# Optimization experiments

Hardware: AMD Instinct MI355X
Metric: run time of the kernel (lower is better)

Reference implementation:

```python
import jax, jax.numpy as jnp
import numpy as np

HIDDEN = 3072
N_HEADS = 16
Q_LORA = 1536
KV_LORA = 512
NOPE = 128
ROPE = 64
QK_HD = NOPE + ROPE  # 192
V_HD = 128
B, S = 2, 1024


def rms_norm(x, w, eps=1e-6):
    xf = x.astype(jnp.float32)
    var = jnp.mean(xf * xf, axis=-1, keepdims=True)
    return w * (xf * jax.lax.rsqrt(var + eps)).astype(x.dtype)


def apply_rope(x):
    # x: (b, s, h, d) with d even; interleaved pair rotation as in the source
    b, s, h, d = x.shape
    pos = jnp.arange(s, dtype=jnp.float32)
    inv_freq = 1.0 / (10000.0 ** (jnp.arange(0, d, 2, dtype=jnp.float32) / d))
    ang = pos[:, None] * inv_freq[None, :]          # (s, d/2)
    sin = jnp.sin(ang)[None, :, None, :]            # (1, s, 1, d/2)
    cos = jnp.cos(ang)[None, :, None, :]
    xr = x.reshape(b, s, h, d // 2, 2)
    x1, x2 = xr[..., 0], xr[..., 1]
    r1 = x1 * cos - x2 * sin
    r2 = x1 * sin + x2 * cos
    return jnp.stack([r1, r2], axis=-1).reshape(b, s, h, d)


def setup_inputs() -> dict:
    key = jax.random.key(0)
    ks = jax.random.split(key, 16)
    sc = 0.02
    inp = {
        "hidden_states": jax.random.normal(ks[0], (B, S, HIDDEN), jnp.float32),
        # causal additive mask (s, t): 0 on/below diagonal, -1e9 above
        "mask": jnp.where(jnp.tril(jnp.ones((S, S), bool)), 0.0, -1e9).astype(jnp.float32),
        "wq_a_w": jax.random.normal(ks[1], (Q_LORA, HIDDEN), jnp.float32) * sc,
        "wq_a_b": jnp.zeros((Q_LORA,), jnp.float32),
        "q_norm_w": jnp.ones((Q_LORA,), jnp.float32),
        "wq_b_w": jax.random.normal(ks[2], (HIDDEN, Q_LORA), jnp.float32) * sc,
        "wq_b_b": jnp.zeros((HIDDEN,), jnp.float32),
        "wkv_a_w": jax.random.normal(ks[3], (KV_LORA + ROPE, HIDDEN), jnp.float32) * sc,
        "wkv_a_b": jnp.zeros((KV_LORA + ROPE,), jnp.float32),
        "kv_norm_w": jnp.ones((KV_LORA,), jnp.float32),
        "wkv_b_w": jax.random.normal(ks[4], (N_HEADS * (NOPE + V_HD), KV_LORA), jnp.float32) * sc,
        "wkv_b_b": jnp.zeros((N_HEADS * (NOPE + V_HD),), jnp.float32),
        "wo_w": jax.random.normal(ks[5], (HIDDEN, N_HEADS * V_HD), jnp.float32) * sc,
        "wo_b": jnp.zeros((HIDDEN,), jnp.float32),
    }
    return inp


def reference(hidden_states, mask, wq_a_w, wq_a_b, q_norm_w, wq_b_w, wq_b_b,
              wkv_a_w, wkv_a_b, kv_norm_w, wkv_b_w, wkv_b_b, wo_w, wo_b):
    b, s, _ = hidden_states.shape
    scale = QK_HD ** (-0.5)

    # low-rank Q projection
    q_lat = hidden_states @ wq_a_w.T + wq_a_b                  # (b,s,q_lora)
    q = rms_norm(q_lat, q_norm_w) @ wq_b_w.T + wq_b_b          # (b,s,hidden)
    q = q.reshape(b, s, N_HEADS, QK_HD)
    q_nope, q_rope = q[..., :NOPE], q[..., NOPE:]
    q_rope = apply_rope(q_rope)
    q = jnp.concatenate([q_nope, q_rope], axis=-1)             # (b,s,h,192)

    # low-rank KV projection with decoupled rope key
    kv = hidden_states @ wkv_a_w.T + wkv_a_b                   # (b,s,kv_lora+rope)
    kv_lat, k_rope = kv[..., :KV_LORA], kv[..., KV_LORA:]
    k_rope = apply_rope(k_rope[:, :, None, :])                 # (b,s,1,64)
    kv = rms_norm(kv_lat, kv_norm_w) @ wkv_b_w.T + wkv_b_b
    kv = kv.reshape(b, s, N_HEADS, NOPE + V_HD)
    k_nope, v = kv[..., :NOPE], kv[..., NOPE:]
    k = jnp.concatenate([k_nope, jnp.broadcast_to(k_rope, (b, s, N_HEADS, ROPE))], axis=-1)

    # naive full attention, fp32 softmax (as in source)
    scores = jnp.einsum('bshd,bthd->bsht', q, k) * scale       # (b,s,h,t)
    scores = scores + mask[None, :, None, :]
    p = jax.nn.softmax(scores.astype(jnp.float32), axis=-1)
    out = jnp.einsum('bsht,bthd->bshd', p, v)                  # (b,s,h,v_hd)
    out = out.reshape(b, s, N_HEADS * V_HD)
    return out @ wo_w.T + wo_b
```

## Files before the change

### kernel.cpp

```cpp
#include <hip/hip_runtime.h>
#include <stdint.h>
#include <stddef.h>

#define NHEADS 16
#define QLORA  1536
#define KVLORA 512
#define QKH    192
#define VH     128
#define BB     2
#define SS     1024
#define MROWS  (BB*SS)
#define HID    3072

typedef __attribute__((ext_vector_type(4))) float fx4;
typedef __attribute__((ext_vector_type(4))) short sx4;
typedef __attribute__((ext_vector_type(8))) short sx8;

__device__ __forceinline__ short f2bf(float f) {
  uint32_t u = __builtin_bit_cast(uint32_t, f);
  u = (u + 0x7fffu + ((u >> 16) & 1u)) >> 16;
  return (short)u;
}
__device__ __forceinline__ float bf2f(short s) {
  uint32_t u = ((uint32_t)(uint16_t)s) << 16;
  return __builtin_bit_cast(float, u);
}
__device__ __forceinline__ void gl_lds16(const void* g, void* l) {
  __builtin_amdgcn_global_load_lds((const __attribute__((address_space(1))) void*)g,
                                   (__attribute__((address_space(3))) void*)l, 16, 0, 0);
}
__device__ __forceinline__ sx8 ldfrag(const short* p) {
  sx4 lo = *(const sx4*)p;
  sx4 hi = *(const sx4*)(p + 16);
  sx8 r;
  r[0]=lo[0]; r[1]=lo[1]; r[2]=lo[2]; r[3]=lo[3];
  r[4]=hi[0]; r[5]=hi[1]; r[6]=hi[2]; r[7]=hi[3];
  return r;
}
__device__ __forceinline__ sx8 ldfrag_swz(const short* lds, int row, int rowShorts,
                                          int baseChunk, int g) {
  const int r7 = row & 7;
  const int gh = g >> 1, lo4 = (g & 1) * 4;
  int ch0 = baseChunk + gh;
  int ch1 = baseChunk + 2 + gh;
  ch0 = (ch0 & ~7) | ((ch0 & 7) ^ r7);
  ch1 = (ch1 & ~7) | ((ch1 & 7) ^ r7);
  const short* base = lds + row * rowShorts;
  sx4 a = *(const sx4*)(base + ch0 * 8 + lo4);
  sx4 b = *(const sx4*)(base + ch1 * 8 + lo4);
  sx8 r;
  r[0]=a[0]; r[1]=a[1]; r[2]=a[2]; r[3]=a[3];
  r[4]=b[0]; r[5]=b[1]; r[6]=b[2]; r[7]=b[3];
  return r;
}

struct CvtSeg { const float* src; short* dst; int n4; };
__global__ void k_cvt6(CvtSeg s0, CvtSeg s1, CvtSeg s2, CvtSeg s3, CvtSeg s4, CvtSeg s5) {
  const CvtSeg segs[6] = {s0, s1, s2, s3, s4, s5};
  const int stride = gridDim.x * blockDim.x;
  const int t0 = blockIdx.x * blockDim.x + threadIdx.x;
#pragma unroll
  for (int s = 0; s < 6; ++s) {
    const float* src = segs[s].src;
    short* dst = segs[s].dst;
    const int n4 = segs[s].n4;
    for (int i = t0; i < n4; i += stride) {
      fx4 v = *(const fx4*)(src + (size_t)i * 4);
      sx4 o;
      o[0] = f2bf(v[0]); o[1] = f2bf(v[1]); o[2] = f2bf(v[2]); o[3] = f2bf(v[3]);
      *(sx4*)(dst + (size_t)i * 4) = o;
    }
  }
}

__global__ void k_rope_tab(float* __restrict__ tab) {
  int i = blockIdx.x * blockDim.x + threadIdx.x;
  if (i >= SS * 32) return;
  int pos = i >> 5, fi = i & 31;
  float inv = powf(10000.0f, -(float)fi / 32.0f);
  float ang = (float)pos * inv;
  tab[i * 2]     = cosf(ang);
  tab[i * 2 + 1] = sinf(ang);
}

struct GemmProb {
  const short* A; const short* Bt; const float* bias; void* C;
  int N; int K;
};

template <int SPLITK>
__global__ __launch_bounds__(256, 4)
void k_gemmS(GemmProb p0, GemmProb p1, int nblk0) {
  int nwg = gridDim.x;
  int bid = (blockIdx.x % 8) * (nwg >> 3) + (blockIdx.x >> 3);
  const GemmProb p = (bid < nblk0) ? p0 : p1;
  int lb = (bid < nblk0) ? bid : bid - nblk0;
  const int N = p.N, K = p.K;
  const int NT = (N + 127) >> 7;
  const int tiles = 16 * NT;
  const int tile = lb % tiles;
  const int pi = (SPLITK > 1) ? (lb / tiles) : 0;
  const int m0 = (tile % 16) * 128;
  const int n0 = (tile / 16) * 128;
  const int Kc = K / SPLITK;
  const int k0 = pi * Kc;

  __shared__ short As[128 * 64];
  __shared__ short Bs[128 * 64];
  const int tid  = threadIdx.x;
  const int lane = tid & 63;
  const int g    = lane >> 4;
  const int r16  = lane & 15;
  const int wave = tid >> 6;
  const int wm   = (wave >> 1) * 64;
  const int wn   = (wave & 1) * 64;

  fx4 acc[4][4] = {};

  for (int kk = k0; kk < k0 + Kc; kk += 64) {
#pragma unroll
    for (int i = 0; i < 4; ++i) {
      int cc  = tid + 256 * i;
      int row = cc >> 3;
      int src = ((cc & 7) ^ (row & 7)) * 8;
      int bn = n0 + row; if (bn > N - 1) bn = N - 1;
      gl_lds16(p.A + (size_t)(m0 + row) * K + kk + src, &As[cc * 8]);
      gl_lds16(p.Bt + (size_t)bn * K + kk + src, &Bs[cc * 8]);
    }
    __syncthreads();

#pragma unroll
    for (int s = 0; s < 2; ++s) {
      sx8 af[4], bfv[4];
#pragma unroll
      for (int mi = 0; mi < 4; ++mi)
        af[mi] = ldfrag_swz(As, wm + mi * 16 + r16, 64, s * 4, g);
#pragma unroll
      for (int ni = 0; ni < 4; ++ni)
        bfv[ni] = ldfrag_swz(Bs, wn + ni * 16 + r16, 64, s * 4, g);
#pragma unroll
      for (int mi = 0; mi < 4; ++mi)
#pragma unroll
        for (int ni = 0; ni < 4; ++ni)
          acc[mi][ni] = __builtin_amdgcn_mfma_f32_16x16x32_bf16(af[mi], bfv[ni], acc[mi][ni], 0, 0, 0);
    }
    __syncthreads();
  }

  if (SPLITK > 1) {
    float* Cp = (float*)p.C + (size_t)pi * 2048 * N;
#pragma unroll
    for (int mi = 0; mi < 4; ++mi) {
      int mbase = m0 + wm + mi * 16 + 4 * g;
#pragma unroll
      for (int ni = 0; ni < 4; ++ni) {
        int ncol = n0 + wn + ni * 16 + r16;
        if (ncol < N) {
#pragma unroll
          for (int r = 0; r < 4; ++r)
            Cp[(size_t)(mbase + r) * N + ncol] = acc[mi][ni][r];
        }
      }
    }
  } else {
#pragma unroll
    for (int mi = 0; mi < 4; ++mi) {
      int mbase = m0 + wm + mi * 16 + 4 * g;
#pragma unroll
      for (int ni = 0; ni < 4; ++ni) {
        int ncol = n0 + wn + ni * 16 + r16;
        if (ncol < N) {
          float bv = p.bias[ncol];
#pragma unroll
          for (int r = 0; r < 4; ++r)
            ((short*)p.C)[(size_t)(mbase + r) * N + ncol] = f2bf(acc[mi][ni][r] + bv);
        }
      }
    }
  }
}

__global__ __launch_bounds__(256)
void k_prep(const float* __restrict__ qp, const float* __restrict__ q_bias,
            const float* __restrict__ q_norm_w, short* __restrict__ qn,
            const float* __restrict__ kvp, const float* __restrict__ kv_bias,
            const float* __restrict__ kv_norm_w, short* __restrict__ kvn,
            short* __restrict__ kr, const float* __restrict__ tab) {
  const int row = blockIdx.x;
  const int t = threadIdx.x;
  const size_t QS = (size_t)2048 * QLORA;
  const size_t KS = (size_t)2048 * 576;

  float x[8];
  float s1 = 0.f, s2 = 0.f;
  if (t < 192) {
    const float* a = qp + (size_t)row * QLORA + t * 8;
    fx4 u0 = *(const fx4*)(a),          u1 = *(const fx4*)(a + 4);
    fx4 v0 = *(const fx4*)(a + QS),     v1 = *(const fx4*)(a + QS + 4);
    fx4 w0 = *(const fx4*)(a + 2 * QS), w1 = *(const fx4*)(a + 2 * QS + 4);
#pragma unroll
    for (int j = 0; j < 4; ++j) {
      x[j]     = u0[j] + v0[j] + w0[j] + q_bias[t * 8 + j];
      x[4 + j] = u1[j] + v1[j] + w1[j] + q_bias[t * 8 + 4 + j];
    }
#pragma unroll
    for (int j = 0; j < 8; ++j) s1 += x[j] * x[j];
  } else {
    const int c = t - 192;
    const float* a = kvp + (size_t)row * 576 + c * 8;
    fx4 u0 = *(const fx4*)(a),          u1 = *(const fx4*)(a + 4);
    fx4 v0 = *(const fx4*)(a + KS),     v1 = *(const fx4*)(a + KS + 4);
    fx4 w0 = *(const fx4*)(a + 2 * KS), w1 = *(const fx4*)(a + 2 * KS + 4);
#pragma unroll
    for (int j = 0; j < 4; ++j) {
      x[j]     = u0[j] + v0[j] + w0[j] + kv_bias[c * 8 + j];
      x[4 + j] = u1[j] + v1[j] + w1[j] + kv_bias[c * 8 + 4 + j];
    }
#pragma unroll
    for (int j = 0; j < 8; ++j) s2 += x[j] * x[j];
  }
#pragma unroll
  for (int o = 32; o >= 1; o >>= 1) {
    s1 += __shfl_xor(s1, o, 64);
    s2 += __shfl_xor(s2, o, 64);
  }
  __shared__ float r1[4], r2[4];
  if ((t & 63) == 0) { r1[t >> 6] = s1; r2[t >> 6] = s2; }
  __syncthreads();
  float qss = r1[0] + r1[1] + r1[2] + r1[3];
  float kss = r2[0] + r2[1] + r2[2] + r2[3];
  float qrs = 1.0f / sqrtf(qss / (float)QLORA + 1e-6f);
  float krs = 1.0f / sqrtf(kss / (float)KVLORA + 1e-6f);

  if (t < 192) {
    sx8 o;
#pragma unroll
    for (int j = 0; j < 8; ++j) o[j] = f2bf(x[j] * qrs * q_norm_w[t * 8 + j]);
    *(sx8*)(qn + (size_t)row * QLORA + t * 8) = o;
  } else {
    int c = t - 192;
    sx8 o;
#pragma unroll
    for (int j = 0; j < 8; ++j) o[j] = f2bf(x[j] * krs * kv_norm_w[c * 8 + j]);
    *(sx8*)(kvn + (size_t)row * KVLORA + c * 8) = o;
  }
  if (t < 8) {
    const float* a = kvp + (size_t)row * 576 + 512 + t * 8;
    fx4 u0 = *(const fx4*)(a),          u1 = *(const fx4*)(a + 4);
    fx4 v0 = *(const fx4*)(a + KS),     v1 = *(const fx4*)(a + KS + 4);
    fx4 w0 = *(const fx4*)(a + 2 * KS), w1 = *(const fx4*)(a + 2 * KS + 4);
    float y[8];
#pragma unroll
    for (int j = 0; j < 4; ++j) {
      y[j]     = u0[j] + v0[j] + w0[j] + kv_bias[512 + t * 8 + j];
      y[4 + j] = u1[j] + v1[j] + w1[j] + kv_bias[512 + t * 8 + 4 + j];
    }
    int pos = row & (SS - 1);
    sx8 o;
#pragma unroll
    for (int k = 0; k < 4; ++k) {
      int i = t * 4 + k;
      float c = tab[(pos * 32 + i) * 2], s = tab[(pos * 32 + i) * 2 + 1];
      o[2 * k]     = f2bf(y[2 * k] * c - y[2 * k + 1] * s);
      o[2 * k + 1] = f2bf(y[2 * k] * s + y[2 * k + 1] * c);
    }
    *(sx8*)(kr + (size_t)row * 64 + t * 8) = o;
  }
}

__global__ __launch_bounds__(256)
void k_post(const short* __restrict__ kvb, short* __restrict__ vt,
            short* __restrict__ qb, const float* __restrict__ tab) {
  const int bid = blockIdx.x;
  const int tid = threadIdx.x;
  if (bid < 512) {
    const int bh = bid >> 4;
    const int t0 = (bid & 15) * 64;
    const int b = bh >> 4, h = bh & 15;
    __shared__ short sm[64 * 128];
#pragma unroll
    for (int i = 0; i < 4; ++i) {
      int c = tid + 256 * i;
      int tt = c >> 4, d0 = (c & 15) * 8;
      sx8 v = *(const sx8*)(kvb + ((size_t)(b * SS + t0 + tt)) * 4096 + h * 256 + 128 + d0);
      *(sx8*)(sm + tt * 128 + d0) = v;
    }
    __syncthreads();
#pragma unroll
    for (int i = 0; i < 4; ++i) {
      int c = tid + 256 * i;
      int d = c >> 3, tof = (c & 7) * 8;
      sx8 v;
#pragma unroll
      for (int j = 0; j < 8; ++j) v[j] = sm[(tof + j) * 128 + d];
      *(sx8*)(vt + ((size_t)bh * VH + d) * SS + t0 + tof) = v;
    }
  } else {
    int p = (bid - 512) * 256 + tid;
    int j = p & 7, h = (p >> 3) & 15, row = p >> 7;
    int pos = row & (SS - 1);
    size_t base = (((size_t)row * NHEADS + h) * QKH) + 128 + j * 8;
    sx8 x = *(const sx8*)(qb + base);
    sx8 o;
#pragma unroll
    for (int k = 0; k < 4; ++k) {
      int i = j * 4 + k;
      float c = tab[(pos * 32 + i) * 2], s = tab[(pos * 32 + i) * 2 + 1];
      float x1 = bf2f(x[2 * k]), x2 = bf2f(x[2 * k + 1]);
      o[2 * k]     = f2bf(x1 * c - x2 * s);
      o[2 * k + 1] = f2bf(x1 * s + x2 * c);
    }
    *(sx8*)(qb + base) = o;
  }
}

__global__ __launch_bounds__(256)
void k_osum(const float* __restrict__ p, const float* __restrict__ bias,
            float* __restrict__ out) {
  const size_t OS = (size_t)2048 * HID;
  int i = blockIdx.x * 256 + threadIdx.x;
  fx4 a = *(const fx4*)(p + (size_t)i * 4);
  fx4 b = *(const fx4*)(p + OS + (size_t)i * 4);
  int col = (i * 4) % HID;
  fx4 bv = *(const fx4*)(bias + col);
  fx4 o = a + b + bv;
  *(fx4*)(out + (size_t)i * 4) = o;
}

__global__ __launch_bounds__(256, 2)
void k_attn(const short* __restrict__ q, const short* __restrict__ kvb,
            const short* __restrict__ kr, const short* __restrict__ vt,
            short* __restrict__ ao) {
  const int bh = blockIdx.x;
  const int b = bh >> 4, h = bh & 15;
  const int qt0 = blockIdx.y * 64;
  const int tid = threadIdx.x;
  const int lane = tid & 63;
  const int wave = tid >> 6;
  const int g = lane >> 4, r16 = lane & 15;
  const int qg = qt0 + wave * 16 + r16;

  __shared__ short Ks[64 * QKH];
  __shared__ short Vs[VH * 64];

  sx8 qf[6];
  {
    const short* qr = q + (((size_t)(b * SS + qg)) * NHEADS + h) * QKH;
#pragma unroll
    for (int f = 0; f < 6; ++f) qf[f] = ldfrag(qr + f * 32 + 4 * g);
  }

  float mrun = -1e30f, lrun = 0.0f;
  fx4 oacc[8] = {};
  const float scale = 0.07216878364870323f;

  const int ntiles = qt0 / 64 + 1;
  for (int kt = 0; kt < ntiles; ++kt) {
    const int t0 = kt * 64;
#pragma unroll
    for (int i = 0; i < 6; ++i) {
      int cc = tid + 256 * i;
      int row = cc / 24, ch = cc % 24;
      int sc = (ch & 24) | ((ch & 7) ^ (row & 7));
      size_t grow = (size_t)(b * SS + t0 + row);
      const short* src = (sc < 16) ? kvb + grow * 4096 + h * 256 + sc * 8
                                   : kr + grow * 64 + (sc - 16) * 8;
      gl_lds16(src, &Ks[cc * 8]);
    }
#pragma unroll
    for (int i = 0; i < 4; ++i) {
      int cc = tid + 256 * i;
      int row = cc >> 3;
      int sc = (cc & 7) ^ (row & 7);
      gl_lds16(vt + ((size_t)bh * VH + row) * SS + t0 + sc * 8, &Vs[cc * 8]);
    }
    __syncthreads();

    const bool diag = (kt == ntiles - 1);
    float pv[16];
    float tmax = -1e30f;
#pragma unroll
    for (int th = 0; th < 4; ++th) {
      fx4 sacc = {};
#pragma unroll
      for (int f = 0; f < 6; ++f) {
        sx8 kf = ldfrag_swz(Ks, th * 16 + r16, QKH, f * 4, g);
        sacc = __builtin_amdgcn_mfma_f32_16x16x32_bf16(kf, qf[f], sacc, 0, 0, 0);
      }
#pragma unroll
      for (int r = 0; r < 4; ++r) {
        int t = t0 + th * 16 + 4 * g + r;
        float s = sacc[r] * scale;
        if (diag && t > qg) s = -1e30f;
        pv[th * 4 + r] = s;
        tmax = fmaxf(tmax, s);
      }
    }
    tmax = fmaxf(tmax, __shfl_xor(tmax, 16, 64));
    tmax = fmaxf(tmax, __shfl_xor(tmax, 32, 64));
    float mnew = fmaxf(mrun, tmax);
    float corr = __expf(mrun - mnew);
    float psum = 0.f;
#pragma unroll
    for (int j = 0; j < 16; ++j) { pv[j] = __expf(pv[j] - mnew); psum += pv[j]; }
    psum += __shfl_xor(psum, 16, 64);
    psum += __shfl_xor(psum, 32, 64);
    lrun = lrun * corr + psum;
    mrun = mnew;
#pragma unroll
    for (int f8 = 0; f8 < 8; ++f8) oacc[f8] *= corr;

    sx8 pf0, pf1;
#pragma unroll
    for (int j = 0; j < 8; ++j) { pf0[j] = f2bf(pv[j]); pf1[j] = f2bf(pv[8 + j]); }

#pragma unroll
    for (int f8 = 0; f8 < 8; ++f8) {
      sx8 v0 = ldfrag_swz(Vs, f8 * 16 + r16, 64, 0, g);
      sx8 v1 = ldfrag_swz(Vs, f8 * 16 + r16, 64, 4, g);
      oacc[f8] = __builtin_amdgcn_mfma_f32_16x16x32_bf16(v0, pf0, oacc[f8], 0, 0, 0);
      oacc[f8] = __builtin_amdgcn_mfma_f32_16x16x32_bf16(v1, pf1, oacc[f8], 0, 0, 0);
    }
    __syncthreads();
  }

  float inv = 1.0f / lrun;
#pragma unroll
  for (int f8 = 0; f8 < 8; ++f8)
#pragma unroll
    for (int r = 0; r < 4; ++r) {
      int d = f8 * 16 + 4 * g + r;
      ao[(((size_t)(b * SS + qg)) * NHEADS + h) * VH + d] = f2bf(oacc[f8][r] * inv);
    }
}

extern "C" void kernel_launch(void* const* d_in, const int* in_sizes, int n_in,
                              void* d_out, int out_size, void* d_ws, size_t ws_size,
                              hipStream_t stream) {
  const float* hs       = (const float*)d_in[0];
  const float* wq_a_w   = (const float*)d_in[2];
  const float* wq_a_b   = (const float*)d_in[3];
  const float* q_norm_w = (const float*)d_in[4];
  const float* wq_b_w   = (const float*)d_in[5];
  const float* wq_b_b   = (const float*)d_in[6];
  const float* wkv_a_w  = (const float*)d_in[7];
  const float* wkv_a_b  = (const float*)d_in[8];
  const float* kv_norm_w= (const float*)d_in[9];
  const float* wkv_b_w  = (const float*)d_in[10];
  const float* wkv_b_b  = (const float*)d_in[11];
  const float* wo_w     = (const float*)d_in[12];
  const float* wo_b     = (const float*)d_in[13];
  float* out = (float*)d_out;

  short* ws0 = (short*)d_ws;
  size_t off = 0;
  short* wqa_bf  = ws0 + off; off += (size_t)QLORA * HID;
  short* wqb_bf  = ws0 + off; off += (size_t)HID * QLORA;
  short* wkva_bf = ws0 + off; off += (size_t)576 * HID;
  short* wkvb_bf = ws0 + off; off += (size_t)4096 * KVLORA;
  short* wo_bf   = ws0 + off; off += (size_t)HID * 2048;
  short* h_bf    = ws0 + off; off += (size_t)MROWS * HID;
  short* qn      = ws0 + off; off += (size_t)MROWS * QLORA;
  short* kvn     = ws0 + off; off += (size_t)MROWS * KVLORA;
  short* kr      = ws0 + off; off += (size_t)MROWS * 64;
  short* qb      = ws0 + off; off += (size_t)MROWS * HID;
  short* kvb     = ws0 + off; off += (size_t)MROWS * 4096;
  short* vtb     = ws0 + off; off += (size_t)BB * NHEADS * VH * SS;
  short* ao      = ws0 + off; off += (size_t)MROWS * 2048;
  float* tab     = (float*)(ws0 + off + (off & 1));
  float* arena   = tab + SS * 64;
  float* qlatp   = arena;
  float* kvp     = arena + (size_t)3 * 2048 * QLORA;
  float* wop     = arena;

  {
    CvtSeg s0{wq_a_w,  wqa_bf,  (int)((size_t)QLORA * HID / 4)};
    CvtSeg s1{wq_b_w,  wqb_bf,  (int)((size_t)HID * QLORA / 4)};
    CvtSeg s2{wkv_a_w, wkva_bf, (int)((size_t)576 * HID / 4)};
    CvtSeg s3{wkv_b_w, wkvb_bf, (int)((size_t)4096 * KVLORA / 4)};
    CvtSeg s4{wo_w,    wo_bf,   (int)((size_t)HID * 2048 / 4)};
    CvtSeg s5{hs,      h_bf,    (int)((size_t)MROWS * HID / 4)};
    k_cvt6<<<2048, 256, 0, stream>>>(s0, s1, s2, s3, s4, s5);
  }
  k_rope_tab<<<(SS * 32 + 255) / 256, 256, 0, stream>>>(tab);

  {
    GemmProb pq{h_bf, wqa_bf,  nullptr, qlatp, QLORA, HID};
    GemmProb pk{h_bf, wkva_bf, nullptr, kvp,   576,   HID};
    int nb0 = 16 * (QLORA / 128) * 3;
    int nb1 = 16 * ((576 + 127) / 128) * 3;
    k_gemmS<3><<<nb0 + nb1, 256, 0, stream>>>(pq, pk, nb0);
  }

  k_prep<<<MROWS, 256, 0, stream>>>(qlatp, wq_a_b, q_norm_w, qn,
                                    kvp, wkv_a_b, kv_norm_w, kvn, kr, tab);

  {
    GemmProb pq{qn,  wqb_bf,  wq_b_b,  qb,  HID,  QLORA};
    GemmProb pk{kvn, wkvb_bf, wkv_b_b, kvb, 4096, KVLORA};
    int nb0 = 16 * (HID / 128);
    int nb1 = 16 * (4096 / 128);
    k_gemmS<1><<<nb0 + nb1, 256, 0, stream>>>(pq, pk, nb0);
  }

  k_post<<<512 + 1024, 256, 0, stream>>>(kvb, vtb, qb, tab);

  k_attn<<<dim3(BB * NHEADS, SS / 64), 256, 0, stream>>>(qb, kvb, kr, vtb, ao);

  {
    GemmProb po{ao, wo_bf, nullptr, wop, HID, 2048};
    int nb = 16 * (HID / 128) * 2;
    k_gemmS<2><<<nb, 256, 0, stream>>>(po, po, nb);
  }
  k_osum<<<(MROWS * HID / 4) / 256, 256, 0, stream>>>(wop, wo_b, out);
}
```

Before: 250.9 us.

## Replace GEMM with 256x256-tile, 8-wave, double-buffered LDS pipelined kernel

```diff
diff --git a/kernel.cpp b/kernel.cpp
--- a/kernel.cpp
+++ b/kernel.cpp
@@ -89,92 +89,145 @@
 };
 
 template <int SPLITK>
-__global__ __launch_bounds__(256, 4)
-void k_gemmS(GemmProb p0, GemmProb p1, int nblk0) {
+__global__ __launch_bounds__(512, 2)
+void k_g8(GemmProb p0, GemmProb p1, int nblk0) {
   int nwg = gridDim.x;
   int bid = (blockIdx.x % 8) * (nwg >> 3) + (blockIdx.x >> 3);
   const GemmProb p = (bid < nblk0) ? p0 : p1;
   int lb = (bid < nblk0) ? bid : bid - nblk0;
   const int N = p.N, K = p.K;
-  const int NT = (N + 127) >> 7;
-  const int tiles = 16 * NT;
+  const int NT = N >> 8;
+  const int tiles = 8 * NT;
   const int tile = lb % tiles;
   const int pi = (SPLITK > 1) ? (lb / tiles) : 0;
-  const int m0 = (tile % 16) * 128;
-  const int n0 = (tile / 16) * 128;
+  const int m0 = (tile & 7) * 256;
+  const int n0 = (tile >> 3) * 256;
   const int Kc = K / SPLITK;
   const int k0 = pi * Kc;
 
-  __shared__ short As[128 * 64];
-  __shared__ short Bs[128 * 64];
+  __shared__ short lds[2][4][128 * 64];
+
   const int tid  = threadIdx.x;
   const int lane = tid & 63;
+  const int wave = tid >> 6;
+  const int wr   = wave >> 2;
+  const int wc   = wave & 3;
   const int g    = lane >> 4;
   const int r16  = lane & 15;
-  const int wave = tid >> 6;
-  const int wm   = (wave >> 1) * 64;
-  const int wn   = (wave & 1) * 64;
-
-  fx4 acc[4][4] = {};
-
-  for (int kk = k0; kk < k0 + Kc; kk += 64) {
-#pragma unroll
-    for (int i = 0; i < 4; ++i) {
-      int cc  = tid + 256 * i;
-      int row = cc >> 3;
-      int src = ((cc & 7) ^ (row & 7)) * 8;
-      int bn = n0 + row; if (bn > N - 1) bn = N - 1;
-      gl_lds16(p.A + (size_t)(m0 + row) * K + kk + src, &As[cc * 8]);
-      gl_lds16(p.Bt + (size_t)bn * K + kk + src, &Bs[cc * 8]);
-    }
-    __syncthreads();
-
-#pragma unroll
-    for (int s = 0; s < 2; ++s) {
-      sx8 af[4], bfv[4];
-#pragma unroll
-      for (int mi = 0; mi < 4; ++mi)
-        af[mi] = ldfrag_swz(As, wm + mi * 16 + r16, 64, s * 4, g);
-#pragma unroll
-      for (int ni = 0; ni < 4; ++ni)
-        bfv[ni] = ldfrag_swz(Bs, wn + ni * 16 + r16, 64, s * 4, g);
-#pragma unroll
-      for (int mi = 0; mi < 4; ++mi)
-#pragma unroll
-        for (int ni = 0; ni < 4; ++ni)
-          acc[mi][ni] = __builtin_amdgcn_mfma_f32_16x16x32_bf16(af[mi], bfv[ni], acc[mi][ni], 0, 0, 0);
-    }
-    __syncthreads();
-  }
+  const int bhalf = 2 + (wc >> 1);
+  const int brow0 = (wc & 1) * 64;
+
+  fx4 acc[8][4] = {};
+
+#define STAGE_HALF(dbuf, h, kk)                                              \
+  do {                                                                       \
+    const short* _b = ((h) < 2) ? p.A : p.Bt;                                \
+    int _rb = ((h) < 2) ? (m0 + (h) * 128) : (n0 + ((h) - 2) * 128);         \
+    _Pragma("unroll")                                                        \
+    for (int _i = 0; _i < 2; ++_i) {                                         \
+      int _cc = tid + 512 * _i;                                              \
+      int _row = _cc >> 3;                                                   \
+      int _src = ((_cc & 7) ^ (_row & 7)) * 8;                               \
+      gl_lds16(_b + (size_t)(_rb + _row) * K + (kk) + _src,                  \
+               &lds[dbuf][h][_cc * 8]);                                      \
+    }                                                                        \
+  } while (0)
+
+#define MFMA16(mh, nh)                                                       \
+  do {                                                                       \
+    __builtin_amdgcn_s_setprio(1);                                           \
+    _Pragma("unroll")                                                        \
+    for (int _mi = 0; _mi < 4; ++_mi)                                        \
+      _Pragma("unroll")                                                      \
+      for (int _ni = 0; _ni < 2; ++_ni)                                      \
+        _Pragma("unroll")                                                    \
+        for (int _s = 0; _s < 2; ++_s)                                       \
+          acc[(mh) * 4 + _mi][(nh) * 2 + _ni] =                              \
+            __builtin_amdgcn_mfma_f32_16x16x32_bf16(                         \
+              af[_mi][_s], bfv[nh][_ni][_s],                                 \
+              acc[(mh) * 4 + _mi][(nh) * 2 + _ni], 0, 0, 0);                 \
+    __builtin_amdgcn_s_setprio(0);                                           \
+  } while (0)
+
+  const int nk = Kc >> 6;
+  STAGE_HALF(0, 0, k0); STAGE_HALF(0, 1, k0);
+  STAGE_HALF(0, 2, k0); STAGE_HALF(0, 3, k0);
+
+  for (int t = 0; t < nk; ++t) {
+    const int buf = t & 1, sbuf = buf ^ 1;
+    const bool pf = (t + 1 < nk);
+    const int kkn = k0 + (t + 1) * 64;
+
+    sx8 af[4][2], bfv[2][2][2];
+
+    if (pf) {
+      STAGE_HALF(sbuf, 0, kkn);
+      asm volatile("s_waitcnt vmcnt(2)" ::: "memory");
+    } else {
+      asm volatile("s_waitcnt vmcnt(0)" ::: "memory");
+    }
+    __builtin_amdgcn_s_barrier();
+    __builtin_amdgcn_sched_barrier(0);
+#pragma unroll
+    for (int nh = 0; nh < 2; ++nh)
+#pragma unroll
+      for (int ni = 0; ni < 2; ++ni)
+#pragma unroll
+        for (int s = 0; s < 2; ++s)
+          bfv[nh][ni][s] = ldfrag_swz(&lds[buf][bhalf][0],
+                                      brow0 + nh * 32 + ni * 16 + r16, 64, s * 4, g);
+#pragma unroll
+    for (int mi = 0; mi < 4; ++mi)
+#pragma unroll
+      for (int s = 0; s < 2; ++s)
+        af[mi][s] = ldfrag_swz(&lds[buf][wr][0], mi * 16 + r16, 64, s * 4, g);
+    MFMA16(0, 0);
+    __builtin_amdgcn_s_barrier();
+
+    if (pf) STAGE_HALF(sbuf, 1, kkn);
+    MFMA16(0, 1);
+    __builtin_amdgcn_s_barrier();
+
+    if (pf) STAGE_HALF(sbuf, 2, kkn);
+#pragma unroll
+    for (int mi = 0; mi < 4; ++mi)
+#pragma unroll
+      for (int s = 0; s < 2; ++s)
+        af[mi][s] = ldfrag_swz(&lds[buf][wr][0], 64 + mi * 16 + r16, 64, s * 4, g);
+    MFMA16(1, 0);
+    __builtin_amdgcn_s_barrier();
+
+    if (pf) STAGE_HALF(sbuf, 3, kkn);
+    MFMA16(1, 1);
+    __builtin_amdgcn_s_barrier();
+  }
+#undef STAGE_HALF
+#undef MFMA16
 
   if (SPLITK > 1) {
     float* Cp = (float*)p.C + (size_t)pi * 2048 * N;
 #pragma unroll
-    for (int mi = 0; mi < 4; ++mi) {
-      int mbase = m0 + wm + mi * 16 + 4 * g;
-#pragma unroll
-      for (int ni = 0; ni < 4; ++ni) {
-        int ncol = n0 + wn + ni * 16 + r16;
-        if (ncol < N) {
-#pragma unroll
-          for (int r = 0; r < 4; ++r)
-            Cp[(size_t)(mbase + r) * N + ncol] = acc[mi][ni][r];
-        }
+    for (int mi8 = 0; mi8 < 8; ++mi8) {
+      int mbase = m0 + wr * 128 + mi8 * 16 + 4 * g;
+#pragma unroll
+      for (int ni4 = 0; ni4 < 4; ++ni4) {
+        int ncol = n0 + wc * 64 + ni4 * 16 + r16;
+#pragma unroll
+        for (int r = 0; r < 4; ++r)
+          Cp[(size_t)(mbase + r) * N + ncol] = acc[mi8][ni4][r];
       }
     }
   } else {
 #pragma unroll
-    for (int mi = 0; mi < 4; ++mi) {
-      int mbase = m0 + wm + mi * 16 + 4 * g;
-#pragma unroll
-      for (int ni = 0; ni < 4; ++ni) {
-        int ncol = n0 + wn + ni * 16 + r16;
-        if (ncol < N) {
-          float bv = p.bias[ncol];
-#pragma unroll
-          for (int r = 0; r < 4; ++r)
-            ((short*)p.C)[(size_t)(mbase + r) * N + ncol] = f2bf(acc[mi][ni][r] + bv);
-        }
+    for (int mi8 = 0; mi8 < 8; ++mi8) {
+      int mbase = m0 + wr * 128 + mi8 * 16 + 4 * g;
+#pragma unroll
+      for (int ni4 = 0; ni4 < 4; ++ni4) {
+        int ncol = n0 + wc * 64 + ni4 * 16 + r16;
+        float bv = p.bias[ncol];
+#pragma unroll
+        for (int r = 0; r < 4; ++r)
+          ((short*)p.C)[(size_t)(mbase + r) * N + ncol] = f2bf(acc[mi8][ni4][r] + bv);
       }
     }
   }
@@ -189,7 +242,7 @@
   const int row = blockIdx.x;
   const int t = threadIdx.x;
   const size_t QS = (size_t)2048 * QLORA;
-  const size_t KS = (size_t)2048 * 576;
+  const size_t KS = (size_t)2048 * 768;
 
   float x[8];
   float s1 = 0.f, s2 = 0.f;
@@ -207,7 +260,7 @@
     for (int j = 0; j < 8; ++j) s1 += x[j] * x[j];
   } else {
     const int c = t - 192;
-    const float* a = kvp + (size_t)row * 576 + c * 8;
+    const float* a = kvp + (size_t)row * 768 + c * 8;
     fx4 u0 = *(const fx4*)(a),          u1 = *(const fx4*)(a + 4);
     fx4 v0 = *(const fx4*)(a + KS),     v1 = *(const fx4*)(a + KS + 4);
     fx4 w0 = *(const fx4*)(a + 2 * KS), w1 = *(const fx4*)(a + 2 * KS + 4);
@@ -245,7 +298,7 @@
     *(sx8*)(kvn + (size_t)row * KVLORA + c * 8) = o;
   }
   if (t < 8) {
-    const float* a = kvp + (size_t)row * 576 + 512 + t * 8;
+    const float* a = kvp + (size_t)row * 768 + 512 + t * 8;
     fx4 u0 = *(const fx4*)(a),          u1 = *(const fx4*)(a + 4);
     fx4 v0 = *(const fx4*)(a + KS),     v1 = *(const fx4*)(a + KS + 4);
     fx4 w0 = *(const fx4*)(a + 2 * KS), w1 = *(const fx4*)(a + 2 * KS + 4);
@@ -456,7 +509,7 @@
   size_t off = 0;
   short* wqa_bf  = ws0 + off; off += (size_t)QLORA * HID;
   short* wqb_bf  = ws0 + off; off += (size_t)HID * QLORA;
-  short* wkva_bf = ws0 + off; off += (size_t)576 * HID;
+  short* wkva_bf = ws0 + off; off += (size_t)768 * HID;
   short* wkvb_bf = ws0 + off; off += (size_t)4096 * KVLORA;
   short* wo_bf   = ws0 + off; off += (size_t)HID * 2048;
   short* h_bf    = ws0 + off; off += (size_t)MROWS * HID;
@@ -486,10 +539,10 @@
 
   {
     GemmProb pq{h_bf, wqa_bf,  nullptr, qlatp, QLORA, HID};
-    GemmProb pk{h_bf, wkva_bf, nullptr, kvp,   576,   HID};
-    int nb0 = 16 * (QLORA / 128) * 3;
-    int nb1 = 16 * ((576 + 127) / 128) * 3;
-    k_gemmS<3><<<nb0 + nb1, 256, 0, stream>>>(pq, pk, nb0);
+    GemmProb pk{h_bf, wkva_bf, nullptr, kvp,   768,   HID};
+    int nb0 = 8 * (QLORA / 256) * 3;
+    int nb1 = 8 * (768 / 256) * 3;
+    k_g8<3><<<nb0 + nb1, 512, 0, stream>>>(pq, pk, nb0);
   }
 
   k_prep<<<MROWS, 256, 0, stream>>>(qlatp, wq_a_b, q_norm_w, qn,
@@ -498,9 +551,9 @@
   {
     GemmProb pq{qn,  wqb_bf,  wq_b_b,  qb,  HID,  QLORA};
     GemmProb pk{kvn, wkvb_bf, wkv_b_b, kvb, 4096, KVLORA};
-    int nb0 = 16 * (HID / 128);
-    int nb1 = 16 * (4096 / 128);
-    k_gemmS<1><<<nb0 + nb1, 256, 0, stream>>>(pq, pk, nb0);
+    int nb0 = 8 * (HID / 256);
+    int nb1 = 8 * (4096 / 256);
+    k_g8<1><<<nb0 + nb1, 512, 0, stream>>>(pq, pk, nb0);
   }
 
   k_post<<<512 + 1024, 256, 0, stream>>>(kvb, vtb, qb, tab);
@@ -509,8 +562,8 @@
 
   {
     GemmProb po{ao, wo_bf, nullptr, wop, HID, 2048};
-    int nb = 16 * (HID / 128) * 2;
-    k_gemmS<2><<<nb, 256, 0, stream>>>(po, po, nb);
+    int nb = 8 * (HID / 256) * 2;
+    k_g8<2><<<nb, 512, 0, stream>>>(po, po, nb);
   }
   k_osum<<<(MROWS * HID / 4) / 256, 256, 0, stream>>>(wop, wo_b, out);
 }
```

Measured after the change: 280.8 us. +11.9%, slower.
